# Performance work log

Hardware: AMD Instinct MI355X
Metric: run time of the kernel (lower is better)

The kernel has to match this reference:

```python
import jax, jax.numpy as jnp
import numpy as np

N_NODES = 1024
N_EDGES = 32768
FEAT = 384
HID = 64
OUT = 64


def setup_inputs() -> dict:
    key = jax.random.key(0)
    ks = jax.random.split(key, 10)
    features = jax.random.normal(ks[0], (N_NODES, FEAT), dtype=jnp.float32)
    edge_index = jax.random.randint(ks[1], (2, N_EDGES), 0, N_NODES, dtype=jnp.int64 if jax.config.jax_enable_x64 else jnp.int32)
    edge_attr = jax.random.uniform(ks[2], (N_EDGES, 1), dtype=jnp.float32)
    # Linear weights (stored as [in, out]; torch Linear does x @ W.T)
    sc = 1.0 / np.sqrt(FEAT)
    Wk = jax.random.uniform(ks[3], (FEAT, HID), dtype=jnp.float32, minval=-sc, maxval=sc)
    Wq = jax.random.uniform(ks[4], (FEAT, HID), dtype=jnp.float32, minval=-sc, maxval=sc)
    Wv = jax.random.uniform(ks[5], (FEAT, OUT), dtype=jnp.float32, minval=-sc, maxval=sc)
    # Embedding tables, init N(0, 1)
    Ek = jax.random.normal(ks[6], (2, HID), dtype=jnp.float32)
    Eq = jax.random.normal(ks[7], (2, HID), dtype=jnp.float32)
    Ev = jax.random.normal(ks[8], (2, OUT), dtype=jnp.float32)
    bias = jnp.full((1,), 0.5, dtype=jnp.float32)
    mult = jnp.full((1,), 10.0, dtype=jnp.float32)
    return {"features": features, "edge_index": edge_index, "edge_attr": edge_attr,
            "Wk": Wk, "Wq": Wq, "Wv": Wv, "Ek": Ek, "Eq": Eq, "Ev": Ev,
            "bias": bias, "mult": mult}


def _dense_adj(src, dst, vals, n, d):
    # torch_geometric.utils.to_dense_adj: scatter-add edge attrs into [N, N, d]
    return jnp.zeros((n, n, d), vals.dtype).at[src, dst].add(vals)


def reference(features, edge_index, edge_attr, Wk, Wq, Wv, Ek, Eq, Ev, bias, mult):
    N, L = features.shape
    k = features @ Wk                      # [N, H]
    q = features @ Wq                      # [N, H]
    v = features @ Wv                      # [N, O]

    # ContinuousEmbeddingIndex: sigmoid interp, weights [E, 2]
    w = jax.nn.sigmoid((edge_attr - bias) * mult)
    w = jnp.concatenate([w, 1.0 - w], axis=-1)

    src, dst = edge_index[0], edge_index[1]
    A = q @ k.T                            # [N, N]

    # key relative embeddings (original casts to int64 -> truncate toward 0)
    rk = jnp.trunc(w @ Ek)                 # [E, H]
    Rk = _dense_adj(src, dst, rk, N, Ek.shape[1])
    A = A + jnp.einsum('ih,ijh->ij', q, Rk)

    # query relative embeddings (also truncated)
    rq = jnp.trunc(w @ Eq)
    Rq = _dense_adj(src, dst, rq, N, Eq.shape[1])
    A = A + jnp.einsum('jh,ijh->ij', k, Rq)

    # term3: (q_repeat * k_repeat).sum(-1) == q @ k.T again
    A = A + q @ k.T

    A = jax.nn.softmax(A / jnp.sqrt(jnp.asarray(L, A.dtype)), axis=-1)
    # dropout is identity at inference
    M = A @ v

    # value relative embeddings (float, no truncation)
    rv = w @ Ev                            # [E, O]
    Rv = _dense_adj(src, dst, rv, N, Ev.shape[1])
    M = M + jnp.einsum('ij,ijd->id', A, Rv)
    return M
```

## Files before the change

kernel.cpp:

```cpp
#include <hip/hip_runtime.h>
#include <math.h>

#define N_NODES 1024
#define N_EDGES 32768
#define FEAT    384
#define INV_S   0.05103103630798287f
#define MAXH    1024

__global__ __launch_bounds__(384) void k_kqv(
        const float* __restrict__ feat,
        const float* __restrict__ Wk, const float* __restrict__ Wq,
        const float* __restrict__ Wv,
        float* __restrict__ q, float* __restrict__ k, float* __restrict__ v) {
    __shared__ float fs[4 * FEAT];
    const int tid = threadIdx.x;
    const int row0 = blockIdx.x * 4;
    ((float4*)fs)[tid] = ((const float4*)(feat + (size_t)row0 * FEAT))[tid];
    __syncthreads();
    const int mat = tid >> 7;
    const int sub = tid & 127;
    const int col = sub & 63;
    const int rh  = sub >> 6;
    const float* W  = (mat == 0) ? Wq : (mat == 1 ? Wk : Wv);
    const float* f0 = fs + (rh * 2) * FEAT;
    const float* f1 = fs + (rh * 2 + 1) * FEAT;
    float a0 = 0.f, a1 = 0.f;
    #pragma unroll 8
    for (int f = 0; f < FEAT; ++f) {
        float wv = W[f * 64 + col];
        a0 = fmaf(f0[f], wv, a0);
        a1 = fmaf(f1[f], wv, a1);
    }
    float* out = (mat == 0) ? q : (mat == 1 ? k : v);
    out[(row0 + rh * 2 + 0) * 64 + col] = a0;
    out[(row0 + rh * 2 + 1) * 64 + col] = a1;
}

__global__ __launch_bounds__(256) void k_qkt(
        const float* __restrict__ q, const float* __restrict__ k,
        float* __restrict__ A) {
    __shared__ float qs[64][65];
    __shared__ float kst[64][65];
    const int tid = threadIdx.x;
    const int rowbase = blockIdx.y * 64, colbase = blockIdx.x * 64;
    for (int idx = tid; idx < 4096; idx += 256) {
        int r = idx >> 6, c = idx & 63;
        qs[r][c] = q[(rowbase + r) * 64 + c];
        kst[c][r] = k[(colbase + r) * 64 + c];
    }
    __syncthreads();
    const int tx = tid & 15, ty = tid >> 4;
    float acc[4][4] = {};
    for (int kk = 0; kk < 64; ++kk) {
        float a0 = qs[ty * 4 + 0][kk], a1 = qs[ty * 4 + 1][kk];
        float a2 = qs[ty * 4 + 2][kk], a3 = qs[ty * 4 + 3][kk];
        float b0 = kst[kk][tx * 4 + 0], b1 = kst[kk][tx * 4 + 1];
        float b2 = kst[kk][tx * 4 + 2], b3 = kst[kk][tx * 4 + 3];
        acc[0][0] = fmaf(a0, b0, acc[0][0]); acc[0][1] = fmaf(a0, b1, acc[0][1]);
        acc[0][2] = fmaf(a0, b2, acc[0][2]); acc[0][3] = fmaf(a0, b3, acc[0][3]);
        acc[1][0] = fmaf(a1, b0, acc[1][0]); acc[1][1] = fmaf(a1, b1, acc[1][1]);
        acc[1][2] = fmaf(a1, b2, acc[1][2]); acc[1][3] = fmaf(a1, b3, acc[1][3]);
        acc[2][0] = fmaf(a2, b0, acc[2][0]); acc[2][1] = fmaf(a2, b1, acc[2][1]);
        acc[2][2] = fmaf(a2, b2, acc[2][2]); acc[2][3] = fmaf(a2, b3, acc[2][3]);
        acc[3][0] = fmaf(a3, b0, acc[3][0]); acc[3][1] = fmaf(a3, b1, acc[3][1]);
        acc[3][2] = fmaf(a3, b2, acc[3][2]); acc[3][3] = fmaf(a3, b3, acc[3][3]);
    }
    for (int i = 0; i < 4; ++i) {
        float4 o = make_float4(2.f * acc[i][0], 2.f * acc[i][1],
                               2.f * acc[i][2], 2.f * acc[i][3]);
        *(float4*)&A[(size_t)(rowbase + ty * 4 + i) * N_NODES + colbase + tx * 4] = o;
    }
}

__global__ __launch_bounds__(512) void k_mega(
        const float* __restrict__ A0, const float* __restrict__ q,
        const float* __restrict__ k, const float* __restrict__ v,
        const int* __restrict__ ei, const float* __restrict__ eattr,
        const float* __restrict__ Ek, const float* __restrict__ Eq,
        const float* __restrict__ Ev,
        const float* __restrict__ bias, const float* __restrict__ mult,
        float* __restrict__ M) {
    __shared__ __align__(16) float As[4][N_NODES];
    __shared__ float qr[4][64];
    __shared__ __align__(16) float scratch[2048];
    __shared__ float redm[8], reds[8];
    __shared__ float sS[4][2];
    __shared__ int nhit;
    int*   list  = (int*)scratch;
    float* wlist = scratch + 1024;
    float* red   = scratch;

    const int tid  = threadIdx.x;
    const int lane = tid & 63;
    const int wave = tid >> 6;
    const int row0 = blockIdx.x * 4;

    if (tid < 8) ((float*)sS)[tid] = 0.f;
    if (tid == 8) nhit = 0;
    __syncthreads();

    {
        const float4* src4 = (const float4*)(A0 + (size_t)row0 * N_NODES);
        #pragma unroll
        for (int i = 0; i < 2; ++i)
            ((float4*)As)[tid + i * 512] = src4[tid + i * 512];
        if (tid < 256) qr[tid >> 6][tid & 63] = q[row0 * 64 + tid];

        const int4* s4 = (const int4*)ei;
        #pragma unroll 4
        for (int it = 0; it < 16; ++it) {
            const int i4 = tid + it * 512;
            const int4 sv = s4[i4];
            const int eb = i4 * 4;
            if ((unsigned)(sv.x - row0) < 4u) { int p = atomicAdd(&nhit, 1); if (p < MAXH) list[p] = eb + 0; }
            if ((unsigned)(sv.y - row0) < 4u) { int p = atomicAdd(&nhit, 1); if (p < MAXH) list[p] = eb + 1; }
            if ((unsigned)(sv.z - row0) < 4u) { int p = atomicAdd(&nhit, 1); if (p < MAXH) list[p] = eb + 2; }
            if ((unsigned)(sv.w - row0) < 4u) { int p = atomicAdd(&nhit, 1); if (p < MAXH) list[p] = eb + 3; }
        }
    }
    __syncthreads();
    const int nh = min(nhit, MAXH);

    {
        const float b0 = bias[0], mu = mult[0];
        const float ek0 = Ek[lane], ek1 = Ek[64 + lane];
        const float eq0 = Eq[lane], eq1 = Eq[64 + lane];
        for (int i = wave; i < nh; i += 8) {
            const int e   = list[i];
            const int src = ei[e], dst = ei[N_EDGES + e];
            const float w  = 1.0f / (1.0f + expf(-(eattr[e] - b0) * mu));
            const float rk = truncf(w * ek0 + (1.0f - w) * ek1);
            const float rq = truncf(w * eq0 + (1.0f - w) * eq1);
            float c = qr[src - row0][lane] * rk + k[(size_t)dst * 64 + lane] * rq;
            #pragma unroll
            for (int off = 32; off >= 1; off >>= 1) c += __shfl_xor(c, off, 64);
            if (lane == 0) {
                atomicAdd(&As[src - row0][dst], c);
                wlist[i] = w;
            }
        }
    }
    __syncthreads();

    const int g  = tid >> 7;
    const int lt = tid & 127;
    {
        float4 x0 = *(float4*)&As[g][lt * 8];
        float4 x1 = *(float4*)&As[g][lt * 8 + 4];
        float m = fmaxf(fmaxf(fmaxf(x0.x, x0.y), fmaxf(x0.z, x0.w)),
                        fmaxf(fmaxf(x1.x, x1.y), fmaxf(x1.z, x1.w)));
        #pragma unroll
        for (int off = 32; off >= 1; off >>= 1) m = fmaxf(m, __shfl_xor(m, off, 64));
        if (lane == 0) redm[wave] = m;
        __syncthreads();
        m = fmaxf(redm[g * 2], redm[g * 2 + 1]);
        float e0 = expf((x0.x - m) * INV_S), e1 = expf((x0.y - m) * INV_S);
        float e2 = expf((x0.z - m) * INV_S), e3 = expf((x0.w - m) * INV_S);
        float e4 = expf((x1.x - m) * INV_S), e5 = expf((x1.y - m) * INV_S);
        float e6 = expf((x1.z - m) * INV_S), e7 = expf((x1.w - m) * INV_S);
        float s = ((e0 + e1) + (e2 + e3)) + ((e4 + e5) + (e6 + e7));
        #pragma unroll
        for (int off = 32; off >= 1; off >>= 1) s += __shfl_xor(s, off, 64);
        if (lane == 0) reds[wave] = s;
        __syncthreads();
        s = reds[g * 2] + reds[g * 2 + 1];
        const float rs = 1.0f / s;
        *(float4*)&As[g][lt * 8]     = make_float4(e0 * rs, e1 * rs, e2 * rs, e3 * rs);
        *(float4*)&As[g][lt * 8 + 4] = make_float4(e4 * rs, e5 * rs, e6 * rs, e7 * rs);
    }
    __syncthreads();

    for (int i = tid; i < nh; i += 512) {
        const int e  = list[i];
        const int rl = ei[e] - row0, dst = ei[N_EDGES + e];
        const float pr = As[rl][dst];
        const float w  = wlist[i];
        atomicAdd(&sS[rl][0], pr * w);
        atomicAdd(&sS[rl][1], pr * (1.0f - w));
    }
    __syncthreads();

    {
        const float* vp = v + (size_t)(wave * 128) * 64 + lane;
        const float* p0 = &As[0][wave * 128];
        const float* p1 = &As[1][wave * 128];
        const float* p2 = &As[2][wave * 128];
        const float* p3 = &As[3][wave * 128];
        float a0 = 0.f, a1 = 0.f, a2 = 0.f, a3 = 0.f;
        #pragma unroll 2
        for (int j4 = 0; j4 < 128; j4 += 4) {
            float4 c0 = *(const float4*)&p0[j4];
            float4 c1 = *(const float4*)&p1[j4];
            float4 c2 = *(const float4*)&p2[j4];
            float4 c3 = *(const float4*)&p3[j4];
            float v0 = vp[(j4 + 0) * 64];
            float v1 = vp[(j4 + 1) * 64];
            float v2 = vp[(j4 + 2) * 64];
            float v3 = vp[(j4 + 3) * 64];
            a0 = fmaf(c0.x, v0, a0); a0 = fmaf(c0.y, v1, a0);
            a0 = fmaf(c0.z, v2, a0); a0 = fmaf(c0.w, v3, a0);
            a1 = fmaf(c1.x, v0, a1); a1 = fmaf(c1.y, v1, a1);
            a1 = fmaf(c1.z, v2, a1); a1 = fmaf(c1.w, v3, a1);
            a2 = fmaf(c2.x, v0, a2); a2 = fmaf(c2.y, v1, a2);
            a2 = fmaf(c2.z, v2, a2); a2 = fmaf(c2.w, v3, a2);
            a3 = fmaf(c3.x, v0, a3); a3 = fmaf(c3.y, v1, a3);
            a3 = fmaf(c3.z, v2, a3); a3 = fmaf(c3.w, v3, a3);
        }
        red[(0 * 8 + wave) * 64 + lane] = a0;
        red[(1 * 8 + wave) * 64 + lane] = a1;
        red[(2 * 8 + wave) * 64 + lane] = a2;
        red[(3 * 8 + wave) * 64 + lane] = a3;
    }
    __syncthreads();
    if (tid < 256) {
        const int r = tid >> 6, d = tid & 63;
        float acc = 0.f;
        #pragma unroll
        for (int w8 = 0; w8 < 8; ++w8) acc += red[(r * 8 + w8) * 64 + d];
        acc += sS[r][0] * Ev[d] + sS[r][1] * Ev[64 + d];
        M[(row0 + r) * 64 + d] = acc;
    }
}

extern "C" void kernel_launch(void* const* d_in, const int* in_sizes, int n_in,
                              void* d_out, int out_size, void* d_ws, size_t ws_size,
                              hipStream_t stream) {
    (void)in_sizes; (void)n_in; (void)out_size; (void)ws_size;
    const float* feat  = (const float*)d_in[0];
    const int*   ei    = (const int*)d_in[1];
    const float* eattr = (const float*)d_in[2];
    const float* Wk    = (const float*)d_in[3];
    const float* Wq    = (const float*)d_in[4];
    const float* Wv    = (const float*)d_in[5];
    const float* Ek    = (const float*)d_in[6];
    const float* Eq    = (const float*)d_in[7];
    const float* Ev    = (const float*)d_in[8];
    const float* bias  = (const float*)d_in[9];
    const float* mult  = (const float*)d_in[10];
    float* M = (float*)d_out;

    float* wsf = (float*)d_ws;
    float* q = wsf;
    float* k = wsf + 65536;
    float* v = wsf + 131072;
    float* A = wsf + 196608;

    k_kqv<<<256, 384, 0, stream>>>(feat, Wk, Wq, Wv, q, k, v);
    k_qkt<<<dim3(16, 16), 256, 0, stream>>>(q, k, A);
    k_mega<<<256, 512, 0, stream>>>(A, q, k, v, ei, eattr, Ek, Eq, Ev,
                                    bias, mult, M);
}
```

Before: 123.8 us.

## Fuse QK^T score computation into the mega kernel, dropping the dense A buffer

```diff
diff --git a/kernel.cpp b/kernel.cpp
--- a/kernel.cpp
+++ b/kernel.cpp
@@ -36,45 +36,9 @@
     out[(row0 + rh * 2 + 1) * 64 + col] = a1;
 }
 
-__global__ __launch_bounds__(256) void k_qkt(
+__global__ __launch_bounds__(512) void k_mega(
         const float* __restrict__ q, const float* __restrict__ k,
-        float* __restrict__ A) {
-    __shared__ float qs[64][65];
-    __shared__ float kst[64][65];
-    const int tid = threadIdx.x;
-    const int rowbase = blockIdx.y * 64, colbase = blockIdx.x * 64;
-    for (int idx = tid; idx < 4096; idx += 256) {
-        int r = idx >> 6, c = idx & 63;
-        qs[r][c] = q[(rowbase + r) * 64 + c];
-        kst[c][r] = k[(colbase + r) * 64 + c];
-    }
-    __syncthreads();
-    const int tx = tid & 15, ty = tid >> 4;
-    float acc[4][4] = {};
-    for (int kk = 0; kk < 64; ++kk) {
-        float a0 = qs[ty * 4 + 0][kk], a1 = qs[ty * 4 + 1][kk];
-        float a2 = qs[ty * 4 + 2][kk], a3 = qs[ty * 4 + 3][kk];
-        float b0 = kst[kk][tx * 4 + 0], b1 = kst[kk][tx * 4 + 1];
-        float b2 = kst[kk][tx * 4 + 2], b3 = kst[kk][tx * 4 + 3];
-        acc[0][0] = fmaf(a0, b0, acc[0][0]); acc[0][1] = fmaf(a0, b1, acc[0][1]);
-        acc[0][2] = fmaf(a0, b2, acc[0][2]); acc[0][3] = fmaf(a0, b3, acc[0][3]);
-        acc[1][0] = fmaf(a1, b0, acc[1][0]); acc[1][1] = fmaf(a1, b1, acc[1][1]);
-        acc[1][2] = fmaf(a1, b2, acc[1][2]); acc[1][3] = fmaf(a1, b3, acc[1][3]);
-        acc[2][0] = fmaf(a2, b0, acc[2][0]); acc[2][1] = fmaf(a2, b1, acc[2][1]);
-        acc[2][2] = fmaf(a2, b2, acc[2][2]); acc[2][3] = fmaf(a2, b3, acc[2][3]);
-        acc[3][0] = fmaf(a3, b0, acc[3][0]); acc[3][1] = fmaf(a3, b1, acc[3][1]);
-        acc[3][2] = fmaf(a3, b2, acc[3][2]); acc[3][3] = fmaf(a3, b3, acc[3][3]);
-    }
-    for (int i = 0; i < 4; ++i) {
-        float4 o = make_float4(2.f * acc[i][0], 2.f * acc[i][1],
-                               2.f * acc[i][2], 2.f * acc[i][3]);
-        *(float4*)&A[(size_t)(rowbase + ty * 4 + i) * N_NODES + colbase + tx * 4] = o;
-    }
-}
-
-__global__ __launch_bounds__(512) void k_mega(
-        const float* __restrict__ A0, const float* __restrict__ q,
-        const float* __restrict__ k, const float* __restrict__ v,
+        const float* __restrict__ v,
         const int* __restrict__ ei, const float* __restrict__ eattr,
         const float* __restrict__ Ek, const float* __restrict__ Eq,
         const float* __restrict__ Ev,
@@ -97,15 +61,10 @@
 
     if (tid < 8) ((float*)sS)[tid] = 0.f;
     if (tid == 8) nhit = 0;
-    __syncthreads();
-
-    {
-        const float4* src4 = (const float4*)(A0 + (size_t)row0 * N_NODES);
-        #pragma unroll
-        for (int i = 0; i < 2; ++i)
-            ((float4*)As)[tid + i * 512] = src4[tid + i * 512];
-        if (tid < 256) qr[tid >> 6][tid & 63] = q[row0 * 64 + tid];
-
+    if (tid < 256) qr[tid >> 6][tid & 63] = q[row0 * 64 + tid];
+    __syncthreads();
+
+    {
         const int4* s4 = (const int4*)ei;
         #pragma unroll 4
         for (int it = 0; it < 16; ++it) {
@@ -117,6 +76,41 @@
             if ((unsigned)(sv.z - row0) < 4u) { int p = atomicAdd(&nhit, 1); if (p < MAXH) list[p] = eb + 2; }
             if ((unsigned)(sv.w - row0) < 4u) { int p = atomicAdd(&nhit, 1); if (p < MAXH) list[p] = eb + 3; }
         }
+    }
+
+    {
+        float qa[4][4];
+        #pragma unroll
+        for (int r = 0; r < 4; ++r)
+            #pragma unroll
+            for (int c = 0; c < 4; ++c) qa[r][c] = 0.f;
+        #pragma unroll
+        for (int jj = 0; jj < 2; ++jj) {
+            const int j = tid + jj * 512;
+            const float4* kj = (const float4*)(k + (size_t)j * 64);
+            float a0 = 0.f, a1 = 0.f, a2 = 0.f, a3 = 0.f;
+            #pragma unroll
+            for (int kk4 = 0; kk4 < 16; ++kk4) {
+                const float4 kv = kj[kk4];
+                const float4 q0 = *(const float4*)&qr[0][kk4 * 4];
+                const float4 q1 = *(const float4*)&qr[1][kk4 * 4];
+                const float4 q2 = *(const float4*)&qr[2][kk4 * 4];
+                const float4 q3 = *(const float4*)&qr[3][kk4 * 4];
+                a0 = fmaf(q0.x, kv.x, a0); a0 = fmaf(q0.y, kv.y, a0);
+                a0 = fmaf(q0.z, kv.z, a0); a0 = fmaf(q0.w, kv.w, a0);
+                a1 = fmaf(q1.x, kv.x, a1); a1 = fmaf(q1.y, kv.y, a1);
+                a1 = fmaf(q1.z, kv.z, a1); a1 = fmaf(q1.w, kv.w, a1);
+                a2 = fmaf(q2.x, kv.x, a2); a2 = fmaf(q2.y, kv.y, a2);
+                a2 = fmaf(q2.z, kv.z, a2); a2 = fmaf(q2.w, kv.w, a2);
+                a3 = fmaf(q3.x, kv.x, a3); a3 = fmaf(q3.y, kv.y, a3);
+                a3 = fmaf(q3.z, kv.z, a3); a3 = fmaf(q3.w, kv.w, a3);
+            }
+            As[0][j] = 2.f * a0;
+            As[1][j] = 2.f * a1;
+            As[2][j] = 2.f * a2;
+            As[3][j] = 2.f * a3;
+        }
+        (void)qa;
     }
     __syncthreads();
     const int nh = min(nhit, MAXH);
@@ -243,10 +237,8 @@
     float* q = wsf;
     float* k = wsf + 65536;
     float* v = wsf + 131072;
-    float* A = wsf + 196608;
 
     k_kqv<<<256, 384, 0, stream>>>(feat, Wk, Wq, Wv, q, k, v);
-    k_qkt<<<dim3(16, 16), 256, 0, stream>>>(q, k, A);
-    k_mega<<<256, 512, 0, stream>>>(A, q, k, v, ei, eattr, Ek, Eq, Ev,
+    k_mega<<<256, 512, 0, stream>>>(q, k, v, ei, eattr, Ek, Eq, Ev,
                                     bias, mult, M);
 }
```

After: 129.0 us. 4.2% more time.
